# Performance work log

Measured on AMD Instinct MI355X. Metric: run time of the kernel, lower is better.

Reference implementation:

```python
import jax, jax.numpy as jnp
import numpy as np

N_VERTICES = 24  # hardcoded via torch.eye(24) in the original
K = 3


def normalized_adj(adj):
    # scipy version: L = (A @ D^-1/2).T @ D^-1/2 = D^-1/2 @ A^T @ D^-1/2
    d = adj.sum(axis=1)
    d_inv_sqrt = jnp.where(d > 0, 1.0 / jnp.sqrt(d), 0.0)
    return (adj * d_inv_sqrt[None, :]).T * d_inv_sqrt[None, :]


def cheb_polynomials(L, k_order):
    Ts = [jnp.eye(N_VERTICES, dtype=L.dtype), L]
    for _ in range(2, k_order):
        Ts.append(2.0 * L @ Ts[-1] - Ts[-2])
    return jnp.stack(Ts[:k_order])  # (K, N, N)


def setup_inputs() -> dict:
    key = jax.random.key(0)
    k1, k2, k3 = jax.random.split(key, 3)
    x = jax.random.normal(k1, (64, 32, N_VERTICES, 512), dtype=jnp.float32)
    adj = jax.random.uniform(k2, (N_VERTICES, N_VERTICES), dtype=jnp.float32)
    Theta = jax.random.normal(k3, (K, 32, 32), dtype=jnp.float32)
    return {"x": x, "adj": adj, "Theta": Theta}


def reference(x, adj, Theta):
    # x: (b, c, n, t); adj: (n, n); Theta: (K, c, o)
    L = normalized_adj(adj)
    T = cheb_polynomials(L, K)  # (K, n, m)
    # original per-timestep, per-k: rhs[b,m,c] = sum_n x[b,n,c] T_k[n,m];
    # out[b,m,o] += rhs @ Theta_k. Fused over t and k, final permute -> (b,o,m,t).
    out = jnp.einsum('knm,bcnt,kco->bomt', T, x, Theta)
    return out
```

## Files before the change

kernel.cpp:

```cpp
#include <hip/hip_runtime.h>
#include <hip/hip_bf16.h>
#include <stdint.h>


#define NV 24
#define CIN 32
#define COUT 32
#define TDIM 512
#define BATCH 64
#define MDIM 768
#define KD 768
#define BM 128
#define BN 128
#define BK 32
#define NKT (KD / BK)
#define NTT (TDIM / BN)
#define NMT (MDIM / BM)
#define BLOB (BM * BK)
#define BSTRIDE 40

typedef __attribute__((ext_vector_type(8))) short short8v;
typedef __attribute__((ext_vector_type(4))) float float4v;

__device__ inline unsigned short f2bf(float f) {
    unsigned int u = __float_as_uint(f);
    unsigned int r = (u + 0x7fffu + ((u >> 16) & 1u)) >> 16;
    return (unsigned short)r;
}

__global__ __launch_bounds__(256) void prep_w(const float* __restrict__ adj,
                                              const float* __restrict__ Theta,
                                              unsigned short* __restrict__ Wp) {
    __shared__ float adjS[NV * NV];
    __shared__ float disS[NV];
    __shared__ float LS[NV * NV];
    __shared__ float T2S[NV * NV];
    int tid = threadIdx.x;
    for (int e = tid; e < NV * NV; e += 256) adjS[e] = adj[e];
    __syncthreads();
    if (tid < NV) {
        float d = 0.f;
        for (int j = 0; j < NV; ++j) d += adjS[tid * NV + j];
        disS[tid] = (d > 0.f) ? rsqrtf(d) : 0.f;
    }
    __syncthreads();
    for (int e = tid; e < NV * NV; e += 256) {
        int i = e / NV, j = e % NV;
        LS[e] = disS[i] * adjS[j * NV + i] * disS[j];
    }
    __syncthreads();
    for (int e = tid; e < NV * NV; e += 256) {
        int i = e / NV, j = e % NV;
        float s = 0.f;
        for (int p = 0; p < NV; ++p) s += LS[i * NV + p] * LS[p * NV + j];
        T2S[e] = 2.f * s - (i == j ? 1.f : 0.f);
    }
    __syncthreads();
    int r0 = blockIdx.x * (MDIM / 64);
    for (int e = tid; e < (MDIM / 64) * KD; e += 256) {
        int lr = e / KD, col = e % KD;
        int row = r0 + lr;
        int o = row / NV, m = row % NV;
        int c = col / NV, n = col % NV;
        float th0 = Theta[0 * CIN * COUT + c * COUT + o];
        float th1 = Theta[1 * CIN * COUT + c * COUT + o];
        float th2 = Theta[2 * CIN * COUT + c * COUT + o];
        float v = (n == m ? th0 : 0.f) + LS[n * NV + m] * th1 + T2S[n * NV + m] * th2;
        size_t idx = (((size_t)(row >> 7) * NKT + (col >> 5)) * BM + (row & 127)) * BK + (col & 31);
        Wp[idx] = f2bf(v);
    }
}

__global__ __launch_bounds__(256, 4) void gemm_fused(const unsigned short* __restrict__ Wp,
                                                     const float* __restrict__ x,
                                                     float* __restrict__ out) {
    __shared__ __attribute__((aligned(16))) unsigned short As[BM * BK];
    __shared__ __attribute__((aligned(16))) unsigned short Bs[BN * BSTRIDE];

    int id = blockIdx.x;
    int hi = id / 48;
    int rem = id - hi * 48;
    int mt = rem >> 3;
    int g = hi * 8 + (rem & 7);
    int b = g >> 2;
    int tt = g & 3;

    int tid = threadIdx.x;
    int wave = tid >> 6;
    int lane = tid & 63;
    int quad = lane >> 4;
    int l16 = lane & 15;
    int wm = wave >> 1, wn = wave & 1;
    int kq = wave;
    int tp = lane;

    const unsigned short* Ab = Wp + (size_t)mt * NKT * BLOB;
    const float* xb = x + (size_t)b * KD * TDIM + tt * BN;

    const float4v zero4 = {0.f, 0.f, 0.f, 0.f};
    float4v acc[4][4];
#pragma unroll
    for (int i = 0; i < 4; ++i)
#pragma unroll
        for (int j = 0; j < 4; ++j) acc[i][j] = zero4;

    uint4 Ar0, Ar1;
    float Xr[16];

    {
        const uint4* ap = (const uint4*)Ab;
        Ar0 = ap[tid];
        Ar1 = ap[tid + 256];
        const float* xr = xb + (size_t)(kq * 8) * TDIM;
#pragma unroll
        for (int kk = 0; kk < 8; ++kk) {
            Xr[kk] = xr[(size_t)kk * TDIM + tp];
            Xr[8 + kk] = xr[(size_t)kk * TDIM + tp + 64];
        }
    }

    for (int kt = 0; kt < NKT; ++kt) {
        union { short8v s; __hip_bfloat162 h[4]; } u0, u1;
#pragma unroll
        for (int i = 0; i < 4; ++i) {
            u0.h[i] = __float22bfloat162_rn({Xr[2 * i], Xr[2 * i + 1]});
            u1.h[i] = __float22bfloat162_rn({Xr[8 + 2 * i], Xr[8 + 2 * i + 1]});
        }
        uint4 a0 = Ar0, a1 = Ar1;

        __syncthreads();
        *(uint4*)(As + tid * 8) = a0;
        *(uint4*)(As + 2048 + tid * 8) = a1;
        *(short8v*)(Bs + tp * BSTRIDE + kq * 8) = u0.s;
        *(short8v*)(Bs + (tp + 64) * BSTRIDE + kq * 8) = u1.s;
        __syncthreads();

        if (kt + 1 < NKT) {
            const uint4* ap = (const uint4*)(Ab + (size_t)(kt + 1) * BLOB);
            Ar0 = ap[tid];
            Ar1 = ap[tid + 256];
            const float* xr = xb + (size_t)((kt + 1) * BK + kq * 8) * TDIM;
#pragma unroll
            for (int kk = 0; kk < 8; ++kk) {
                Xr[kk] = xr[(size_t)kk * TDIM + tp];
                Xr[8 + kk] = xr[(size_t)kk * TDIM + tp + 64];
            }
        }

        short8v a[4], bb[4];
#pragma unroll
        for (int i = 0; i < 4; ++i)
            a[i] = *(const short8v*)(As + (wm * 64 + i * 16 + l16) * BK + quad * 8);
#pragma unroll
        for (int j = 0; j < 4; ++j)
            bb[j] = *(const short8v*)(Bs + (wn * 64 + j * 16 + l16) * BSTRIDE + quad * 8);
#pragma unroll
        for (int i = 0; i < 4; ++i)
#pragma unroll
            for (int j = 0; j < 4; ++j)
                acc[i][j] = __builtin_amdgcn_mfma_f32_16x16x32_bf16(a[i], bb[j], acc[i][j], 0, 0, 0);
    }

    float* outB = out + (size_t)b * MDIM * TDIM;
    int rbase = mt * BM + wm * 64;
    int cbase = tt * BN + wn * 64;
#pragma unroll
    for (int i = 0; i < 4; ++i) {
#pragma unroll
        for (int j = 0; j < 4; ++j) {
            int row0 = rbase + i * 16 + quad * 4;
            int col = cbase + j * 16 + l16;
#pragma unroll
            for (int r = 0; r < 4; ++r)
                outB[(size_t)(row0 + r) * TDIM + col] = acc[i][j][r];
        }
    }
}

extern "C" void kernel_launch(void* const* d_in, const int* in_sizes, int n_in,
                              void* d_out, int out_size, void* d_ws, size_t ws_size,
                              hipStream_t stream) {
    const float* x = (const float*)d_in[0];
    const float* adj = (const float*)d_in[1];
    const float* Theta = (const float*)d_in[2];
    float* out = (float*)d_out;

    unsigned short* Wp = (unsigned short*)d_ws;

    prep_w<<<64, 256, 0, stream>>>(adj, Theta, Wp);
    gemm_fused<<<NMT * NTT * BATCH, 256, 0, stream>>>(Wp, x, out);
}
```

Measured before the change: 221.2 us.

## Load weight fragments directly from global and double-buffer the x tile in LDS

prep_w now writes the bf16 weight matrix pre-swizzled into MFMA fragment order, so each wave loads its A operands straight from global memory into registers and the A tile no longer goes through shared memory. The B (x) tile in LDS is double-buffered, and the next tile's conversion and store happen after the MFMAs, which leaves one barrier per k-step instead of two. The intent is less LDS traffic and fewer barriers. In exchange, A loads are issued in the same iteration they are used, so their latency is exposed, and the launch-bounds occupancy hint is dropped.

```diff
diff --git a/kernel.cpp b/kernel.cpp
--- a/kernel.cpp
+++ b/kernel.cpp
@@ -16,8 +16,8 @@
 #define NKT (KD / BK)
 #define NTT (TDIM / BN)
 #define NMT (MDIM / BM)
-#define BLOB (BM * BK)
 #define BSTRIDE 40
+#define BSSZ (BN * BSTRIDE)
 
 typedef __attribute__((ext_vector_type(8))) short short8v;
 typedef __attribute__((ext_vector_type(4))) float float4v;
@@ -30,7 +30,7 @@
 
 __global__ __launch_bounds__(256) void prep_w(const float* __restrict__ adj,
                                               const float* __restrict__ Theta,
-                                              unsigned short* __restrict__ Wp) {
+                                              unsigned short* __restrict__ WF) {
     __shared__ float adjS[NV * NV];
     __shared__ float disS[NV];
     __shared__ float LS[NV * NV];
@@ -56,26 +56,30 @@
         T2S[e] = 2.f * s - (i == j ? 1.f : 0.f);
     }
     __syncthreads();
-    int r0 = blockIdx.x * (MDIM / 64);
-    for (int e = tid; e < (MDIM / 64) * KD; e += 256) {
-        int lr = e / KD, col = e % KD;
-        int row = r0 + lr;
-        int o = row / NV, m = row % NV;
-        int c = col / NV, n = col % NV;
+    const int TOT = 12 * NKT * 4 * 64 * 8;
+    for (int idx = blockIdx.x * 256 + tid; idx < TOT; idx += 64 * 256) {
+        int e = idx & 7;
+        int lane = (idx >> 3) & 63;
+        int i = (idx >> 9) & 3;
+        int f = idx >> 11;
+        int kt = f % NKT;
+        int mw = f / NKT;
+        int m = mw * 64 + i * 16 + (lane & 15);
+        int k = kt * BK + (lane >> 4) * 8 + e;
+        int o = m / NV, mv = m % NV;
+        int c = k / NV, n = k % NV;
         float th0 = Theta[0 * CIN * COUT + c * COUT + o];
         float th1 = Theta[1 * CIN * COUT + c * COUT + o];
         float th2 = Theta[2 * CIN * COUT + c * COUT + o];
-        float v = (n == m ? th0 : 0.f) + LS[n * NV + m] * th1 + T2S[n * NV + m] * th2;
-        size_t idx = (((size_t)(row >> 7) * NKT + (col >> 5)) * BM + (row & 127)) * BK + (col & 31);
-        Wp[idx] = f2bf(v);
-    }
-}
-
-__global__ __launch_bounds__(256, 4) void gemm_fused(const unsigned short* __restrict__ Wp,
-                                                     const float* __restrict__ x,
-                                                     float* __restrict__ out) {
-    __shared__ __attribute__((aligned(16))) unsigned short As[BM * BK];
-    __shared__ __attribute__((aligned(16))) unsigned short Bs[BN * BSTRIDE];
+        float v = (n == mv ? th0 : 0.f) + LS[n * NV + mv] * th1 + T2S[n * NV + mv] * th2;
+        WF[idx] = f2bf(v);
+    }
+}
+
+__global__ __launch_bounds__(256) void gemm_fused(const unsigned short* __restrict__ WF,
+                                                  const float* __restrict__ x,
+                                                  float* __restrict__ out) {
+    __shared__ __attribute__((aligned(16))) unsigned short Bs[2 * BSSZ];
 
     int id = blockIdx.x;
     int hi = id / 48;
@@ -91,11 +95,12 @@
     int quad = lane >> 4;
     int l16 = lane & 15;
     int wm = wave >> 1, wn = wave & 1;
+    int mw = mt * 2 + wm;
     int kq = wave;
     int tp = lane;
 
-    const unsigned short* Ab = Wp + (size_t)mt * NKT * BLOB;
     const float* xb = x + (size_t)b * KD * TDIM + tt * BN;
+    const short8v* af = (const short8v*)(WF) + (size_t)mw * NKT * 256 + lane;
 
     const float4v zero4 = {0.f, 0.f, 0.f, 0.f};
     float4v acc[4][4];
@@ -104,41 +109,34 @@
 #pragma unroll
         for (int j = 0; j < 4; ++j) acc[i][j] = zero4;
 
-    uint4 Ar0, Ar1;
     float Xr[16];
 
     {
-        const uint4* ap = (const uint4*)Ab;
-        Ar0 = ap[tid];
-        Ar1 = ap[tid + 256];
         const float* xr = xb + (size_t)(kq * 8) * TDIM;
 #pragma unroll
         for (int kk = 0; kk < 8; ++kk) {
             Xr[kk] = xr[(size_t)kk * TDIM + tp];
             Xr[8 + kk] = xr[(size_t)kk * TDIM + tp + 64];
         }
-    }
-
-    for (int kt = 0; kt < NKT; ++kt) {
         union { short8v s; __hip_bfloat162 h[4]; } u0, u1;
 #pragma unroll
         for (int i = 0; i < 4; ++i) {
             u0.h[i] = __float22bfloat162_rn({Xr[2 * i], Xr[2 * i + 1]});
             u1.h[i] = __float22bfloat162_rn({Xr[8 + 2 * i], Xr[8 + 2 * i + 1]});
         }
-        uint4 a0 = Ar0, a1 = Ar1;
-
-        __syncthreads();
-        *(uint4*)(As + tid * 8) = a0;
-        *(uint4*)(As + 2048 + tid * 8) = a1;
         *(short8v*)(Bs + tp * BSTRIDE + kq * 8) = u0.s;
         *(short8v*)(Bs + (tp + 64) * BSTRIDE + kq * 8) = u1.s;
+    }
+
+    for (int kt = 0; kt < NKT; ++kt) {
+        int p = kt & 1;
         __syncthreads();
 
+        short8v a4[4];
+#pragma unroll
+        for (int i = 0; i < 4; ++i) a4[i] = af[(kt * 4 + i) * 64];
+
         if (kt + 1 < NKT) {
-            const uint4* ap = (const uint4*)(Ab + (size_t)(kt + 1) * BLOB);
-            Ar0 = ap[tid];
-            Ar1 = ap[tid + 256];
             const float* xr = xb + (size_t)((kt + 1) * BK + kq * 8) * TDIM;
 #pragma unroll
             for (int kk = 0; kk < 8; ++kk) {
@@ -147,18 +145,29 @@
             }
         }
 
-        short8v a[4], bb[4];
+        const unsigned short* bsr = Bs + p * BSSZ;
+        short8v bb[4];
+#pragma unroll
+        for (int j = 0; j < 4; ++j)
+            bb[j] = *(const short8v*)(bsr + (wn * 64 + j * 16 + l16) * BSTRIDE + quad * 8);
+
 #pragma unroll
         for (int i = 0; i < 4; ++i)
-            a[i] = *(const short8v*)(As + (wm * 64 + i * 16 + l16) * BK + quad * 8);
-#pragma unroll
-        for (int j = 0; j < 4; ++j)
-            bb[j] = *(const short8v*)(Bs + (wn * 64 + j * 16 + l16) * BSTRIDE + quad * 8);
-#pragma unroll
-        for (int i = 0; i < 4; ++i)
 #pragma unroll
             for (int j = 0; j < 4; ++j)
-                acc[i][j] = __builtin_amdgcn_mfma_f32_16x16x32_bf16(a[i], bb[j], acc[i][j], 0, 0, 0);
+                acc[i][j] = __builtin_amdgcn_mfma_f32_16x16x32_bf16(a4[i], bb[j], acc[i][j], 0, 0, 0);
+
+        if (kt + 1 < NKT) {
+            union { short8v s; __hip_bfloat162 h[4]; } u0, u1;
+#pragma unroll
+            for (int i = 0; i < 4; ++i) {
+                u0.h[i] = __float22bfloat162_rn({Xr[2 * i], Xr[2 * i + 1]});
+                u1.h[i] = __float22bfloat162_rn({Xr[8 + 2 * i], Xr[8 + 2 * i + 1]});
+            }
+            unsigned short* bsw = Bs + (p ^ 1) * BSSZ;
+            *(short8v*)(bsw + tp * BSTRIDE + kq * 8) = u0.s;
+            *(short8v*)(bsw + (tp + 64) * BSTRIDE + kq * 8) = u1.s;
+        }
     }
 
     float* outB = out + (size_t)b * MDIM * TDIM;
@@ -185,8 +194,8 @@
     const float* Theta = (const float*)d_in[2];
     float* out = (float*)d_out;
 
-    unsigned short* Wp = (unsigned short*)d_ws;
-
-    prep_w<<<64, 256, 0, stream>>>(adj, Theta, Wp);
-    gemm_fused<<<NMT * NTT * BATCH, 256, 0, stream>>>(Wp, x, out);
-}
+    unsigned short* WF = (unsigned short*)d_ws;
+
+    prep_w<<<64, 256, 0, stream>>>(adj, Theta, WF);
+    gemm_fused<<<NMT * NTT * BATCH, 256, 0, stream>>>(WF, x, out);
+}
```

Result: slower. 230.4 us (+4.1%).
